# Kernel tuning notes

Hardware: AMD Instinct MI355X
Metric: run time of the kernel (lower is better)

Reference implementation:

```python
import jax, jax.numpy as jnp
import numpy as np

BIG = 1e30  # stands in for sys.maxsize in fp32-safe form


def _find_neg_anchors(e_actv, host):
    # Full pairwise Euclidean distance matrix (equivalent to the
    # pdist -> triangular reconstruction in the torch code).
    sq = jnp.sum(e_actv * e_actv, axis=1)                       # [n]
    d2 = sq[:, None] + sq[None, :] - 2.0 * (e_actv @ e_actv.T)  # [n, n]
    dist = jnp.sqrt(jnp.maximum(d2, 0.0))
    n = e_actv.shape[0]
    # mask: self (diagonal) and same-discriminator pairs -> huge distance
    same_discr = host[:, None] == host[None, :]
    eye = jnp.eye(n, dtype=bool)
    dist = jnp.where(same_discr | eye, BIG, dist)
    idxs = jnp.argmin(dist, axis=1)                             # [n]
    return e_actv[idxs]                                         # gather


def setup_inputs() -> dict:
    key = jax.random.key(0)
    k1, k2, k3 = jax.random.split(key, 3)
    n, d = 8192, 256
    e_actv = jax.random.normal(k1, (n, d), dtype=jnp.float32)
    e_ap = jax.random.normal(k2, (n, d), dtype=jnp.float32)
    host = jax.random.randint(k3, (n,), 0, 64, dtype=jnp.int64 if jax.config.read('jax_enable_x64') else jnp.int32)
    return {"e_actv": e_actv, "e_ap": e_ap, "host": host}


def reference(e_actv, e_ap, host):
    # forward returns (e_actv, e_ap, e_an); e_an computed under no_grad
    e_an = jax.lax.stop_gradient(_find_neg_anchors(e_actv, host))
    return (e_actv, e_ap, e_an)
```

## Files before the change

kernel.cpp:

```cpp
#include <hip/hip_runtime.h>
#include <hip/hip_bf16.h>
#include <cmath>
#include <cstddef>

#define N 8192
#define D 256
#define BI 128
#define NT (N / BI)
#define NTRI (NT * (NT + 1) / 2)

typedef __attribute__((ext_vector_type(8))) short short8;
typedef __attribute__((ext_vector_type(4))) float float4v;

__device__ inline ushort f2bf(float x) {
    __hip_bfloat16 h = __float2bfloat16(x);
    return __builtin_bit_cast(ushort, h);
}
__device__ inline float bf2f(ushort u) {
    __hip_bfloat16 h = __builtin_bit_cast(__hip_bfloat16, u);
    return __bfloat162float(h);
}

__device__ inline unsigned long long packKI(float k, int idx) {
    unsigned u = __float_as_uint(k);
    u = (u & 0x80000000u) ? ~u : (u | 0x80000000u);
    return ((unsigned long long)u << 32) | (unsigned)idx;
}

__device__ inline int triT(int t) { return t * (129 - t) / 2; }


__global__ void prep_kernel(const float4* __restrict__ a, const float4* __restrict__ p,
                            float4* __restrict__ out, float* __restrict__ sq,
                            ushort* __restrict__ Ehi, ushort* __restrict__ Elo,
                            unsigned long long* __restrict__ M) {
    const int gsz = gridDim.x * blockDim.x;
    const int g0 = blockIdx.x * blockDim.x + threadIdx.x;
    const int total = N * D / 4;

    for (int idx = g0; idx < total; idx += gsz) {
        float4 v = a[idx];
        out[idx] = v;
        float s = v.x * v.x + v.y * v.y + v.z * v.z + v.w * v.w;
        #pragma unroll
        for (int off = 32; off; off >>= 1) s += __shfl_down(s, off);
        if ((threadIdx.x & 63) == 0) sq[idx >> 6] = s;
    }
    for (int idx = g0; idx < total; idx += gsz) out[total + idx] = p[idx];

    {
        const int w = g0 >> 6;
        if (w < 4096) {
            const int lane = threadIdx.x & 63;
            const int tx = lane & 15;
            const int q  = lane >> 4;
            const int r16 = w >> 3;
            const int ktc = w & 7;
            const int row = r16 * 16 + tx;
            const float4 v0 = a[row * 64 + ktc * 8 + q * 2];
            const float4 v1 = a[row * 64 + ktc * 8 + q * 2 + 1];
            float e[8] = {v0.x, v0.y, v0.z, v0.w, v1.x, v1.y, v1.z, v1.w};
            short8 hs, ls;
            #pragma unroll
            for (int j = 0; j < 8; j++) {
                ushort h = f2bf(e[j]);
                ushort l = f2bf(e[j] - bf2f(h));
                hs[j] = (short)h;
                ls[j] = (short)l;
            }
            const size_t off = (size_t)(r16 * 8 + ktc) * 512 + lane * 8;
            *(short8*)&Ehi[off] = hs;
            *(short8*)&Elo[off] = ls;
        }
    }
    for (int i = g0; i < N; i += gsz) M[i] = 0xFFFFFFFFFFFFFFFFull;
}

__launch_bounds__(256, 2)
__global__ void argmin_sym(const ushort* __restrict__ Ehi, const ushort* __restrict__ Elo,
                           const int* __restrict__ host, const float* __restrict__ sq,
                           unsigned long long* __restrict__ M) {
    const int b0 = blockIdx.x;
    const int b = (b0 & 7) * (NTRI / 8) + (b0 >> 3);
    int ti = (int)floor(64.5 - sqrt(64.5 * 64.5 - 2.0 * (double)b));
    while (triT(ti + 1) <= b) ti++;
    while (triT(ti) > b) ti--;
    const int tj = ti + (b - triT(ti));

    __shared__ float sqA_s[BI], sqB_s[BI];
    __shared__ int   hostB_s[BI];
    __shared__ float rowV[2 * BI]; __shared__ int rowI[2 * BI];
    __shared__ float colV[2 * BI]; __shared__ int colI[2 * BI];

    const int ib0 = ti * BI;
    const int jb0 = tj * BI;
    const int tid = threadIdx.x;
    const int lane = tid & 63;
    const int wave = tid >> 6;
    const int wrow = wave >> 1;
    const int wcol = wave & 1;
    const int tx = lane & 15;
    const int q  = lane >> 4;

    if (tid < BI) {
        sqA_s[tid] = sq[ib0 + tid];
        sqB_s[tid] = sq[jb0 + tid];
        hostB_s[tid] = host[jb0 + tid];
    }

    unsigned hostAp[4];
    #pragma unroll
    for (int rt = 0; rt < 4; rt++) {
        unsigned p = 0;
        #pragma unroll
        for (int reg = 0; reg < 4; reg++) {
            int hv = host[ib0 + wrow * 64 + rt * 16 + q * 4 + reg];
            p |= ((unsigned)hv & 0xFFu) << (8 * reg);
        }
        hostAp[rt] = p;
    }

    float4v acc[4][4];
    #pragma unroll
    for (int rt = 0; rt < 4; rt++)
        #pragma unroll
        for (int ct = 0; ct < 4; ct++) acc[rt][ct] = (float4v)(0.0f);

    const int pA = (ib0 >> 4) + wrow * 4;
    const int pB = (jb0 >> 4) + wcol * 4;
    const int lo8 = lane * 8;

    #pragma unroll
    for (int ktc = 0; ktc < 8; ktc++) {
        short8 ah[4], al[4], bh[4], bl[4];
        #pragma unroll
        for (int rt = 0; rt < 4; rt++) {
            const int o = ((pA + rt) * 8 + ktc) * 512 + lo8;
            ah[rt] = *(const short8*)&Ehi[o];
            al[rt] = *(const short8*)&Elo[o];
        }
        #pragma unroll
        for (int ct = 0; ct < 4; ct++) {
            const int o = ((pB + ct) * 8 + ktc) * 512 + lo8;
            bh[ct] = *(const short8*)&Ehi[o];
            bl[ct] = *(const short8*)&Elo[o];
        }
        #pragma unroll
        for (int rt = 0; rt < 4; rt++)
            #pragma unroll
            for (int ct = 0; ct < 4; ct++)
                acc[rt][ct] = __builtin_amdgcn_mfma_f32_16x16x32_bf16(ah[rt], bh[ct], acc[rt][ct], 0, 0, 0);
        #pragma unroll
        for (int rt = 0; rt < 4; rt++)
            #pragma unroll
            for (int ct = 0; ct < 4; ct++)
                acc[rt][ct] = __builtin_amdgcn_mfma_f32_16x16x32_bf16(ah[rt], bl[ct], acc[rt][ct], 0, 0, 0);
        #pragma unroll
        for (int rt = 0; rt < 4; rt++)
            #pragma unroll
            for (int ct = 0; ct < 4; ct++)
                acc[rt][ct] = __builtin_amdgcn_mfma_f32_16x16x32_bf16(al[rt], bh[ct], acc[rt][ct], 0, 0, 0);
    }

    __syncthreads();

    #pragma unroll
    for (int rt = 0; rt < 4; rt++) {
        unsigned hp = hostAp[rt];
        #pragma unroll
        for (int reg = 0; reg < 4; reg++) {
            int il = wrow * 64 + rt * 16 + q * 4 + reg;
            int ig = ib0 + il;
            int ha = (int)((hp >> (8 * reg)) & 0xFFu);
            float v = 3.0e38f; int ix = 0x7fffffff;
            #pragma unroll
            for (int ct = 0; ct < 4; ct++) {
                int jl = wcol * 64 + ct * 16 + tx;
                int jg = jb0 + jl;
                float key = sqB_s[jl] - 2.0f * acc[rt][ct][reg];
                bool masked = (hostB_s[jl] == ha) || (jg == ig);
                if (!masked && (key < v || (key == v && jg < ix))) { v = key; ix = jg; }
            }
            #pragma unroll
            for (int d = 1; d < 16; d <<= 1) {
                float ov = __shfl_xor(v, d);
                int   oi = __shfl_xor(ix, d);
                if (ov < v || (ov == v && oi < ix)) { v = ov; ix = oi; }
            }
            if (tx == 0) { rowV[il * 2 + wcol] = v; rowI[il * 2 + wcol] = ix; }
        }
    }

    if (ti != tj) {
        #pragma unroll
        for (int ct = 0; ct < 4; ct++) {
            int jl = wcol * 64 + ct * 16 + tx;
            int hb = hostB_s[jl];
            float v = 3.0e38f; int ix = 0x7fffffff;
            #pragma unroll
            for (int rt = 0; rt < 4; rt++) {
                unsigned hp = hostAp[rt];
                #pragma unroll
                for (int reg = 0; reg < 4; reg++) {
                    int il = wrow * 64 + rt * 16 + q * 4 + reg;
                    int ig = ib0 + il;
                    bool masked = ((int)((hp >> (8 * reg)) & 0xFFu) == hb);
                    float key = sqA_s[il] - 2.0f * acc[rt][ct][reg];
                    if (!masked && (key < v || (key == v && ig < ix))) { v = key; ix = ig; }
                }
            }
            #pragma unroll
            for (int d = 16; d < 64; d <<= 1) {
                float ov = __shfl_xor(v, d);
                int   oi = __shfl_xor(ix, d);
                if (ov < v || (ov == v && oi < ix)) { v = ov; ix = oi; }
            }
            if (q == 0) { colV[jl * 2 + wrow] = v; colI[jl * 2 + wrow] = ix; }
        }
    }

    __syncthreads();
    if (tid < BI) {
        float v0 = rowV[tid * 2];     int x0 = rowI[tid * 2];
        float v1 = rowV[tid * 2 + 1]; int x1 = rowI[tid * 2 + 1];
        if (v1 < v0 || (v1 == v0 && x1 < x0)) { v0 = v1; x0 = x1; }
        atomicMin(&M[ib0 + tid], packKI(v0, x0));
        if (ti != tj) {
            float w0 = colV[tid * 2];     int y0 = colI[tid * 2];
            float w1 = colV[tid * 2 + 1]; int y1 = colI[tid * 2 + 1];
            if (w1 < w0 || (w1 == w0 && y1 < y0)) { w0 = w1; y0 = y1; }
            atomicMin(&M[jb0 + tid], packKI(w0, y0));
        }
    }
}

__global__ void finalize_kernel(const unsigned long long* __restrict__ M,
                                const float* __restrict__ E, float* __restrict__ out_an) {
    int row = blockIdx.x;
    int t = threadIdx.x;
    int idx = (int)(unsigned)(M[row] & 0xFFFFFFFFull);
    float4 v = *(const float4*)&E[(size_t)idx * D + t * 4];
    *(float4*)&out_an[(size_t)row * D + t * 4] = v;
}

extern "C" void kernel_launch(void* const* d_in, const int* in_sizes, int n_in,
                              void* d_out, int out_size, void* d_ws, size_t ws_size,
                              hipStream_t stream) {
    const float* e_actv = (const float*)d_in[0];
    const float* e_ap   = (const float*)d_in[1];
    const int*   host   = (const int*)d_in[2];
    float* out = (float*)d_out;

    unsigned long long* M = (unsigned long long*)d_ws;
    float*  sq  = (float*)(M + N);
    ushort* Ehi = (ushort*)(sq + N);
    ushort* Elo = Ehi + (size_t)N * D;

    prep_kernel<<<1024, 256, 0, stream>>>(
        (const float4*)e_actv, (const float4*)e_ap, (float4*)out,
        sq, Ehi, Elo, M);
    argmin_sym<<<NTRI, 256, 0, stream>>>(Ehi, Elo, host, sq, M);
    finalize_kernel<<<N, 64, 0, stream>>>(M, e_actv, out + 2 * (size_t)N * D);
}
```

Before: 185.3 us.

## Software-pipeline global fragment loads ahead of MFMA issue in Gram loop

```diff
diff --git a/kernel.cpp b/kernel.cpp
--- a/kernel.cpp
+++ b/kernel.cpp
@@ -130,36 +130,47 @@
     const int pB = (jb0 >> 4) + wcol * 4;
     const int lo8 = lane * 8;
 
-    #pragma unroll
-    for (int ktc = 0; ktc < 8; ktc++) {
-        short8 ah[4], al[4], bh[4], bl[4];
-        #pragma unroll
-        for (int rt = 0; rt < 4; rt++) {
-            const int o = ((pA + rt) * 8 + ktc) * 512 + lo8;
-            ah[rt] = *(const short8*)&Ehi[o];
-            al[rt] = *(const short8*)&Elo[o];
-        }
+    short8 aH[3], aL[3];
+    short8 bhv[2][4], blv[2][4];
+
+    auto loadA = [&](int s) {
+        const int k = s >> 2, rt = s & 3, sl = s % 3;
+        const int o = ((pA + rt) * 8 + k) * 512 + lo8;
+        aH[sl] = *(const short8*)&Ehi[o];
+        aL[sl] = *(const short8*)&Elo[o];
+    };
+    auto loadB = [&](int k) {
+        const int p = k & 1;
         #pragma unroll
         for (int ct = 0; ct < 4; ct++) {
-            const int o = ((pB + ct) * 8 + ktc) * 512 + lo8;
-            bh[ct] = *(const short8*)&Ehi[o];
-            bl[ct] = *(const short8*)&Elo[o];
-        }
-        #pragma unroll
-        for (int rt = 0; rt < 4; rt++)
-            #pragma unroll
-            for (int ct = 0; ct < 4; ct++)
-                acc[rt][ct] = __builtin_amdgcn_mfma_f32_16x16x32_bf16(ah[rt], bh[ct], acc[rt][ct], 0, 0, 0);
-        #pragma unroll
-        for (int rt = 0; rt < 4; rt++)
-            #pragma unroll
-            for (int ct = 0; ct < 4; ct++)
-                acc[rt][ct] = __builtin_amdgcn_mfma_f32_16x16x32_bf16(ah[rt], bl[ct], acc[rt][ct], 0, 0, 0);
-        #pragma unroll
-        for (int rt = 0; rt < 4; rt++)
-            #pragma unroll
-            for (int ct = 0; ct < 4; ct++)
-                acc[rt][ct] = __builtin_amdgcn_mfma_f32_16x16x32_bf16(al[rt], bh[ct], acc[rt][ct], 0, 0, 0);
+            const int o = ((pB + ct) * 8 + k) * 512 + lo8;
+            bhv[p][ct] = *(const short8*)&Ehi[o];
+            blv[p][ct] = *(const short8*)&Elo[o];
+        }
+    };
+
+    loadB(0);
+    loadA(0);
+    loadA(1);
+
+    #pragma unroll
+    for (int s = 0; s < 32; s++) {
+        const int k = s >> 2;
+        const int rt = s & 3;
+        const int sl = s % 3;
+        const int p = k & 1;
+        if (rt == 0 && k < 7) loadB(k + 1);
+        if (s + 2 < 32) loadA(s + 2);
+        __builtin_amdgcn_sched_barrier(0);
+        #pragma unroll
+        for (int ct = 0; ct < 4; ct++)
+            acc[rt][ct] = __builtin_amdgcn_mfma_f32_16x16x32_bf16(aH[sl], bhv[p][ct], acc[rt][ct], 0, 0, 0);
+        #pragma unroll
+        for (int ct = 0; ct < 4; ct++)
+            acc[rt][ct] = __builtin_amdgcn_mfma_f32_16x16x32_bf16(aH[sl], blv[p][ct], acc[rt][ct], 0, 0, 0);
+        #pragma unroll
+        for (int ct = 0; ct < 4; ct++)
+            acc[rt][ct] = __builtin_amdgcn_mfma_f32_16x16x32_bf16(aL[sl], bhv[p][ct], acc[rt][ct], 0, 0, 0);
     }
 
     __syncthreads();
```

Result: no change. 188.0 us (+1.5%).

## Use 128x64 upper-triangular tiles with double-buffered operand loads

Applied to the files above, without the earlier changes.

```diff
diff --git a/kernel.cpp b/kernel.cpp
--- a/kernel.cpp
+++ b/kernel.cpp
@@ -5,9 +5,10 @@
 
 #define N 8192
 #define D 256
-#define BI 128
-#define NT (N / BI)
-#define NTRI (NT * (NT + 1) / 2)
+#define BIR 128
+#define BJC 64
+#define NBI (N / BIR)
+#define NBLK 4160
 
 typedef __attribute__((ext_vector_type(8))) short short8;
 typedef __attribute__((ext_vector_type(4))) float float4v;
@@ -27,7 +28,7 @@
     return ((unsigned long long)u << 32) | (unsigned)idx;
 }
 
-__device__ inline int triT(int t) { return t * (129 - t) / 2; }
+__device__ inline int bandS(int t) { return t * (129 - t); }
 
 
 __global__ void prep_kernel(const float4* __restrict__ a, const float4* __restrict__ p,
@@ -76,24 +77,25 @@
     for (int i = g0; i < N; i += gsz) M[i] = 0xFFFFFFFFFFFFFFFFull;
 }
 
-__launch_bounds__(256, 2)
+__launch_bounds__(256, 3)
 __global__ void argmin_sym(const ushort* __restrict__ Ehi, const ushort* __restrict__ Elo,
                            const int* __restrict__ host, const float* __restrict__ sq,
                            unsigned long long* __restrict__ M) {
     const int b0 = blockIdx.x;
-    const int b = (b0 & 7) * (NTRI / 8) + (b0 >> 3);
-    int ti = (int)floor(64.5 - sqrt(64.5 * 64.5 - 2.0 * (double)b));
-    while (triT(ti + 1) <= b) ti++;
-    while (triT(ti) > b) ti--;
-    const int tj = ti + (b - triT(ti));
-
-    __shared__ float sqA_s[BI], sqB_s[BI];
-    __shared__ int   hostB_s[BI];
-    __shared__ float rowV[2 * BI]; __shared__ int rowI[2 * BI];
-    __shared__ float colV[2 * BI]; __shared__ int colI[2 * BI];
-
-    const int ib0 = ti * BI;
-    const int jb0 = tj * BI;
+    const int b = (b0 & 7) * (NBLK / 8) + (b0 >> 3);
+    int ti = (int)floor((129.0 - sqrt(129.0 * 129.0 - 4.0 * (double)b)) * 0.5);
+    while (bandS(ti + 1) <= b) ti++;
+    while (bandS(ti) > b) ti--;
+    const int tj = 2 * ti + (b - bandS(ti));
+
+    __shared__ float sqA_s[BIR];
+    __shared__ float sqB_s[BJC];
+    __shared__ int   hostB_s[BJC];
+    __shared__ float rowV[2 * BIR]; __shared__ int rowI[2 * BIR];
+    __shared__ float colV[2 * BJC]; __shared__ int colI[2 * BJC];
+
+    const int ib0 = ti * BIR;
+    const int jb0 = tj * BJC;
     const int tid = threadIdx.x;
     const int lane = tid & 63;
     const int wave = tid >> 6;
@@ -102,8 +104,8 @@
     const int tx = lane & 15;
     const int q  = lane >> 4;
 
-    if (tid < BI) {
-        sqA_s[tid] = sq[ib0 + tid];
+    if (tid < BIR) sqA_s[tid] = sq[ib0 + tid];
+    if (tid < BJC) {
         sqB_s[tid] = sq[jb0 + tid];
         hostB_s[tid] = host[jb0 + tid];
     }
@@ -120,46 +122,58 @@
         hostAp[rt] = p;
     }
 
-    float4v acc[4][4];
+    float4v acc[4][2];
     #pragma unroll
     for (int rt = 0; rt < 4; rt++)
         #pragma unroll
-        for (int ct = 0; ct < 4; ct++) acc[rt][ct] = (float4v)(0.0f);
+        for (int ct = 0; ct < 2; ct++) acc[rt][ct] = (float4v)(0.0f);
 
     const int pA = (ib0 >> 4) + wrow * 4;
-    const int pB = (jb0 >> 4) + wcol * 4;
+    const int pB = (jb0 >> 4) + wcol * 2;
     const int lo8 = lane * 8;
 
-    #pragma unroll
-    for (int ktc = 0; ktc < 8; ktc++) {
-        short8 ah[4], al[4], bh[4], bl[4];
+    short8 aH[2][4], aL[2][4], bH[2][2], bL[2][2];
+
+    auto loadChunk = [&](int k) {
+        const int s = k & 1;
         #pragma unroll
         for (int rt = 0; rt < 4; rt++) {
-            const int o = ((pA + rt) * 8 + ktc) * 512 + lo8;
-            ah[rt] = *(const short8*)&Ehi[o];
-            al[rt] = *(const short8*)&Elo[o];
-        }
-        #pragma unroll
-        for (int ct = 0; ct < 4; ct++) {
-            const int o = ((pB + ct) * 8 + ktc) * 512 + lo8;
-            bh[ct] = *(const short8*)&Ehi[o];
-            bl[ct] = *(const short8*)&Elo[o];
-        }
+            const int o = ((pA + rt) * 8 + k) * 512 + lo8;
+            aH[s][rt] = *(const short8*)&Ehi[o];
+            aL[s][rt] = *(const short8*)&Elo[o];
+        }
+        #pragma unroll
+        for (int ct = 0; ct < 2; ct++) {
+            const int o = ((pB + ct) * 8 + k) * 512 + lo8;
+            bH[s][ct] = *(const short8*)&Ehi[o];
+            bL[s][ct] = *(const short8*)&Elo[o];
+        }
+    };
+
+    loadChunk(0);
+    loadChunk(1);
+
+    #pragma unroll
+    for (int k = 0; k < 8; k++) {
+        const int s = k & 1;
+        __builtin_amdgcn_sched_barrier(0);
         #pragma unroll
         for (int rt = 0; rt < 4; rt++)
             #pragma unroll
-            for (int ct = 0; ct < 4; ct++)
-                acc[rt][ct] = __builtin_amdgcn_mfma_f32_16x16x32_bf16(ah[rt], bh[ct], acc[rt][ct], 0, 0, 0);
+            for (int ct = 0; ct < 2; ct++)
+                acc[rt][ct] = __builtin_amdgcn_mfma_f32_16x16x32_bf16(aH[s][rt], bH[s][ct], acc[rt][ct], 0, 0, 0);
         #pragma unroll
         for (int rt = 0; rt < 4; rt++)
             #pragma unroll
-            for (int ct = 0; ct < 4; ct++)
-                acc[rt][ct] = __builtin_amdgcn_mfma_f32_16x16x32_bf16(ah[rt], bl[ct], acc[rt][ct], 0, 0, 0);
+            for (int ct = 0; ct < 2; ct++)
+                acc[rt][ct] = __builtin_amdgcn_mfma_f32_16x16x32_bf16(aH[s][rt], bL[s][ct], acc[rt][ct], 0, 0, 0);
         #pragma unroll
         for (int rt = 0; rt < 4; rt++)
             #pragma unroll
-            for (int ct = 0; ct < 4; ct++)
-                acc[rt][ct] = __builtin_amdgcn_mfma_f32_16x16x32_bf16(al[rt], bh[ct], acc[rt][ct], 0, 0, 0);
+            for (int ct = 0; ct < 2; ct++)
+                acc[rt][ct] = __builtin_amdgcn_mfma_f32_16x16x32_bf16(aL[s][rt], bH[s][ct], acc[rt][ct], 0, 0, 0);
+        __builtin_amdgcn_sched_barrier(0);
+        if (k + 2 < 8) loadChunk(k + 2);
     }
 
     __syncthreads();
@@ -174,11 +188,11 @@
             int ha = (int)((hp >> (8 * reg)) & 0xFFu);
             float v = 3.0e38f; int ix = 0x7fffffff;
             #pragma unroll
-            for (int ct = 0; ct < 4; ct++) {
-                int jl = wcol * 64 + ct * 16 + tx;
+            for (int ct = 0; ct < 2; ct++) {
+                int jl = wcol * 32 + ct * 16 + tx;
                 int jg = jb0 + jl;
                 float key = sqB_s[jl] - 2.0f * acc[rt][ct][reg];
-                bool masked = (hostB_s[jl] == ha) || (jg == ig);
+                bool masked = (hostB_s[jl] == ha) || (jg <= ig);
                 if (!masked && (key < v || (key == v && jg < ix))) { v = key; ix = jg; }
             }
             #pragma unroll
@@ -191,46 +205,45 @@
         }
     }
 
-    if (ti != tj) {
-        #pragma unroll
-        for (int ct = 0; ct < 4; ct++) {
-            int jl = wcol * 64 + ct * 16 + tx;
-            int hb = hostB_s[jl];
-            float v = 3.0e38f; int ix = 0x7fffffff;
-            #pragma unroll
-            for (int rt = 0; rt < 4; rt++) {
-                unsigned hp = hostAp[rt];
-                #pragma unroll
-                for (int reg = 0; reg < 4; reg++) {
-                    int il = wrow * 64 + rt * 16 + q * 4 + reg;
-                    int ig = ib0 + il;
-                    bool masked = ((int)((hp >> (8 * reg)) & 0xFFu) == hb);
-                    float key = sqA_s[il] - 2.0f * acc[rt][ct][reg];
-                    if (!masked && (key < v || (key == v && ig < ix))) { v = key; ix = ig; }
-                }
-            }
-            #pragma unroll
-            for (int d = 16; d < 64; d <<= 1) {
-                float ov = __shfl_xor(v, d);
-                int   oi = __shfl_xor(ix, d);
-                if (ov < v || (ov == v && oi < ix)) { v = ov; ix = oi; }
-            }
-            if (q == 0) { colV[jl * 2 + wrow] = v; colI[jl * 2 + wrow] = ix; }
-        }
+    #pragma unroll
+    for (int ct = 0; ct < 2; ct++) {
+        int jl = wcol * 32 + ct * 16 + tx;
+        int jg = jb0 + jl;
+        int hb = hostB_s[jl];
+        float v = 3.0e38f; int ix = 0x7fffffff;
+        #pragma unroll
+        for (int rt = 0; rt < 4; rt++) {
+            unsigned hp = hostAp[rt];
+            #pragma unroll
+            for (int reg = 0; reg < 4; reg++) {
+                int il = wrow * 64 + rt * 16 + q * 4 + reg;
+                int ig = ib0 + il;
+                bool masked = ((int)((hp >> (8 * reg)) & 0xFFu) == hb) || (ig >= jg);
+                float key = sqA_s[il] - 2.0f * acc[rt][ct][reg];
+                if (!masked && (key < v || (key == v && ig < ix))) { v = key; ix = ig; }
+            }
+        }
+        #pragma unroll
+        for (int d = 16; d < 64; d <<= 1) {
+            float ov = __shfl_xor(v, d);
+            int   oi = __shfl_xor(ix, d);
+            if (ov < v || (ov == v && oi < ix)) { v = ov; ix = oi; }
+        }
+        if (q == 0) { colV[jl * 2 + wrow] = v; colI[jl * 2 + wrow] = ix; }
     }
 
     __syncthreads();
-    if (tid < BI) {
+    if (tid < BIR) {
         float v0 = rowV[tid * 2];     int x0 = rowI[tid * 2];
         float v1 = rowV[tid * 2 + 1]; int x1 = rowI[tid * 2 + 1];
         if (v1 < v0 || (v1 == v0 && x1 < x0)) { v0 = v1; x0 = x1; }
         atomicMin(&M[ib0 + tid], packKI(v0, x0));
-        if (ti != tj) {
-            float w0 = colV[tid * 2];     int y0 = colI[tid * 2];
-            float w1 = colV[tid * 2 + 1]; int y1 = colI[tid * 2 + 1];
-            if (w1 < w0 || (w1 == w0 && y1 < y0)) { w0 = w1; y0 = y1; }
-            atomicMin(&M[jb0 + tid], packKI(w0, y0));
-        }
+    }
+    if (tid < BJC) {
+        float w0 = colV[tid * 2];     int y0 = colI[tid * 2];
+        float w1 = colV[tid * 2 + 1]; int y1 = colI[tid * 2 + 1];
+        if (w1 < w0 || (w1 == w0 && y1 < y0)) { w0 = w1; y0 = y1; }
+        atomicMin(&M[jb0 + tid], packKI(w0, y0));
     }
 }
 
@@ -259,6 +272,6 @@
     prep_kernel<<<1024, 256, 0, stream>>>(
         (const float4*)e_actv, (const float4*)e_ap, (float4*)out,
         sq, Ehi, Elo, M);
-    argmin_sym<<<NTRI, 256, 0, stream>>>(Ehi, Elo, host, sq, M);
+    argmin_sym<<<NBLK, 256, 0, stream>>>(Ehi, Elo, host, sq, M);
     finalize_kernel<<<N, 64, 0, stream>>>(M, e_actv, out + 2 * (size_t)N * D);
 }
```

After: 182.1 us. Within noise of the previous version (-1.7%).

## Restructure symmetric argmin into 64-row strips over four column tiles with register-resident A

Applied to the files above, without the earlier changes.

```diff
diff --git a/kernel.cpp b/kernel.cpp
--- a/kernel.cpp
+++ b/kernel.cpp
@@ -5,12 +5,14 @@
 
 #define N 8192
 #define D 256
-#define BI 128
-#define NT (N / BI)
-#define NTRI (NT * (NT + 1) / 2)
+#define NBB 128
+#define JT 4
+#define NBLK2 2112
 
 typedef __attribute__((ext_vector_type(8))) short short8;
 typedef __attribute__((ext_vector_type(4))) float float4v;
+
+#define U64MAX 0xFFFFFFFFFFFFFFFFull
 
 __device__ inline ushort f2bf(float x) {
     __hip_bfloat16 h = __float2bfloat16(x);
@@ -26,8 +28,11 @@
     u = (u & 0x80000000u) ? ~u : (u | 0x80000000u);
     return ((unsigned long long)u << 32) | (unsigned)idx;
 }
-
-__device__ inline int triT(int t) { return t * (129 - t) / 2; }
+__device__ inline unsigned long long min64(unsigned long long a, unsigned long long b) {
+    return a < b ? a : b;
+}
+
+__device__ inline int segG(int n) { int a = n >> 2, r = n & 3; return 2 * a * (a + 1) + r * (a + 1); }
 
 
 __global__ void prep_kernel(const float4* __restrict__ a, const float4* __restrict__ p,
@@ -76,161 +81,144 @@
     for (int i = g0; i < N; i += gsz) M[i] = 0xFFFFFFFFFFFFFFFFull;
 }
 
-__launch_bounds__(256, 2)
+__launch_bounds__(256, 3)
 __global__ void argmin_sym(const ushort* __restrict__ Ehi, const ushort* __restrict__ Elo,
                            const int* __restrict__ host, const float* __restrict__ sq,
                            unsigned long long* __restrict__ M) {
     const int b0 = blockIdx.x;
-    const int b = (b0 & 7) * (NTRI / 8) + (b0 >> 3);
-    int ti = (int)floor(64.5 - sqrt(64.5 * 64.5 - 2.0 * (double)b));
-    while (triT(ti + 1) <= b) ti++;
-    while (triT(ti) > b) ti--;
-    const int tj = ti + (b - triT(ti));
-
-    __shared__ float sqA_s[BI], sqB_s[BI];
-    __shared__ int   hostB_s[BI];
-    __shared__ float rowV[2 * BI]; __shared__ int rowI[2 * BI];
-    __shared__ float colV[2 * BI]; __shared__ int colI[2 * BI];
-
-    const int ib0 = ti * BI;
-    const int jb0 = tj * BI;
+    const int b = (b0 & 7) * (NBLK2 / 8) + (b0 >> 3);
+    int bb = 0;
+    while (bb < 127 && (NBLK2 - segG(NBB - (bb + 1))) <= b) bb++;
+    const int seg = b - (NBLK2 - segG(NBB - bb));
+    const int tj0 = bb + 4 * seg;
+    const int ntiles = min(JT, NBB - tj0);
+    const int jr0 = tj0 * 64;
+
+    __shared__ float sqB_s[256];
+    __shared__ int   hostB_s[256];
+    __shared__ unsigned long long colV[4][256];
+
     const int tid = threadIdx.x;
     const int lane = tid & 63;
-    const int wave = tid >> 6;
-    const int wrow = wave >> 1;
-    const int wcol = wave & 1;
+    const int w = tid >> 6;
     const int tx = lane & 15;
     const int q  = lane >> 4;
 
-    if (tid < BI) {
-        sqA_s[tid] = sq[ib0 + tid];
-        sqB_s[tid] = sq[jb0 + tid];
-        hostB_s[tid] = host[jb0 + tid];
-    }
-
-    unsigned hostAp[4];
-    #pragma unroll
-    for (int rt = 0; rt < 4; rt++) {
-        unsigned p = 0;
-        #pragma unroll
-        for (int reg = 0; reg < 4; reg++) {
-            int hv = host[ib0 + wrow * 64 + rt * 16 + q * 4 + reg];
-            p |= ((unsigned)hv & 0xFFu) << (8 * reg);
-        }
-        hostAp[rt] = p;
-    }
-
-    float4v acc[4][4];
-    #pragma unroll
-    for (int rt = 0; rt < 4; rt++)
-        #pragma unroll
-        for (int ct = 0; ct < 4; ct++) acc[rt][ct] = (float4v)(0.0f);
-
-    const int pA = (ib0 >> 4) + wrow * 4;
-    const int pB = (jb0 >> 4) + wcol * 4;
+    const int ig0 = bb * 64 + w * 16;
+    const int rg  = bb * 4 + w;
     const int lo8 = lane * 8;
 
-    #pragma unroll
-    for (int ktc = 0; ktc < 8; ktc++) {
-        short8 ah[4], al[4], bh[4], bl[4];
-        #pragma unroll
-        for (int rt = 0; rt < 4; rt++) {
-            const int o = ((pA + rt) * 8 + ktc) * 512 + lo8;
-            ah[rt] = *(const short8*)&Ehi[o];
-            al[rt] = *(const short8*)&Elo[o];
-        }
+    short8 bH[2][4], bL[2][4];
+    auto loadB = [&](int slot, int tj, int k) {
         #pragma unroll
         for (int ct = 0; ct < 4; ct++) {
-            const int o = ((pB + ct) * 8 + ktc) * 512 + lo8;
-            bh[ct] = *(const short8*)&Ehi[o];
-            bl[ct] = *(const short8*)&Elo[o];
-        }
-        #pragma unroll
-        for (int rt = 0; rt < 4; rt++)
+            const int o = ((tj * 4 + ct) * 8 + k) * 512 + lo8;
+            bH[slot][ct] = *(const short8*)&Ehi[o];
+            bL[slot][ct] = *(const short8*)&Elo[o];
+        }
+    };
+    loadB(0, tj0, 0);
+
+    short8 aH[8], aL[8];
+    #pragma unroll
+    for (int k = 0; k < 8; k++) {
+        const int o = (rg * 8 + k) * 512 + lo8;
+        aH[k] = *(const short8*)&Ehi[o];
+        aL[k] = *(const short8*)&Elo[o];
+    }
+
+    float sqA[4];
+    unsigned hostAp = 0;
+    #pragma unroll
+    for (int reg = 0; reg < 4; reg++) {
+        const int ig = ig0 + q * 4 + reg;
+        sqA[reg] = sq[ig];
+        hostAp |= ((unsigned)host[ig] & 0xFFu) << (8 * reg);
+    }
+
+    {
+        const int jcl = min(jr0 + tid, N - 1);
+        if (tid < 256) {
+            sqB_s[tid] = sq[jcl];
+            hostB_s[tid] = host[jcl];
+            #pragma unroll
+            for (int i = 0; i < 4; i++) colV[i][tid] = U64MAX;
+        }
+    }
+    __syncthreads();
+
+    unsigned long long rmin[4] = {U64MAX, U64MAX, U64MAX, U64MAX};
+
+    float4v acc[4];
+    #pragma unroll
+    for (int ct = 0; ct < 4; ct++) acc[ct] = (float4v)(0.0f);
+
+    for (int it = 0; it < ntiles; ++it) {
+        const int tj = tj0 + it;
+        const bool diag = (it == 0) && (seg == 0);
+
+        #pragma unroll
+        for (int k = 0; k < 8; k++) {
+            const int slot = k & 1;
+            if (k < 7) loadB(slot ^ 1, tj, k + 1);
+            else if (it + 1 < ntiles) loadB(slot ^ 1, tj + 1, 0);
+            __builtin_amdgcn_sched_barrier(0);
             #pragma unroll
             for (int ct = 0; ct < 4; ct++)
-                acc[rt][ct] = __builtin_amdgcn_mfma_f32_16x16x32_bf16(ah[rt], bh[ct], acc[rt][ct], 0, 0, 0);
-        #pragma unroll
-        for (int rt = 0; rt < 4; rt++)
+                acc[ct] = __builtin_amdgcn_mfma_f32_16x16x32_bf16(aH[k], bH[slot][ct], acc[ct], 0, 0, 0);
             #pragma unroll
             for (int ct = 0; ct < 4; ct++)
-                acc[rt][ct] = __builtin_amdgcn_mfma_f32_16x16x32_bf16(ah[rt], bl[ct], acc[rt][ct], 0, 0, 0);
-        #pragma unroll
-        for (int rt = 0; rt < 4; rt++)
+                acc[ct] = __builtin_amdgcn_mfma_f32_16x16x32_bf16(aH[k], bL[slot][ct], acc[ct], 0, 0, 0);
             #pragma unroll
             for (int ct = 0; ct < 4; ct++)
-                acc[rt][ct] = __builtin_amdgcn_mfma_f32_16x16x32_bf16(al[rt], bh[ct], acc[rt][ct], 0, 0, 0);
+                acc[ct] = __builtin_amdgcn_mfma_f32_16x16x32_bf16(aL[k], bH[slot][ct], acc[ct], 0, 0, 0);
+        }
+
+        #pragma unroll
+        for (int ct = 0; ct < 4; ct++) {
+            const int jl = it * 64 + ct * 16 + tx;
+            const int jg = jr0 + jl;
+            const float sb = sqB_s[jl];
+            const int   hb = hostB_s[jl];
+            unsigned long long cm = U64MAX;
+            #pragma unroll
+            for (int reg = 0; reg < 4; reg++) {
+                const int ig = ig0 + q * 4 + reg;
+                const int ha = (int)((hostAp >> (8 * reg)) & 0xFFu);
+                const float d = acc[ct][reg];
+                const bool masked = (hb == ha) || (diag && (jg <= ig));
+                const float rkey = fmaf(-2.0f, d, sb);
+                const float ckey = fmaf(-2.0f, d, sqA[reg]);
+                const unsigned long long rp = masked ? U64MAX : packKI(rkey, jg);
+                const unsigned long long cp = masked ? U64MAX : packKI(ckey, ig);
+                rmin[reg] = min64(rmin[reg], rp);
+                cm = min64(cm, cp);
+            }
+            cm = min64(cm, (unsigned long long)__shfl_xor((unsigned long long)cm, 16));
+            cm = min64(cm, (unsigned long long)__shfl_xor((unsigned long long)cm, 32));
+            if (q == 0) colV[w][jl] = cm;
+        }
+        #pragma unroll
+        for (int ct = 0; ct < 4; ct++) acc[ct] = (float4v)(0.0f);
+    }
+
+    #pragma unroll
+    for (int reg = 0; reg < 4; reg++) {
+        #pragma unroll
+        for (int d = 1; d < 16; d <<= 1)
+            rmin[reg] = min64(rmin[reg], (unsigned long long)__shfl_xor((unsigned long long)rmin[reg], d));
+    }
+    if (tx == 0) {
+        #pragma unroll
+        for (int reg = 0; reg < 4; reg++)
+            atomicMin(&M[ig0 + q * 4 + reg], rmin[reg]);
     }
 
     __syncthreads();
-
-    #pragma unroll
-    for (int rt = 0; rt < 4; rt++) {
-        unsigned hp = hostAp[rt];
-        #pragma unroll
-        for (int reg = 0; reg < 4; reg++) {
-            int il = wrow * 64 + rt * 16 + q * 4 + reg;
-            int ig = ib0 + il;
-            int ha = (int)((hp >> (8 * reg)) & 0xFFu);
-            float v = 3.0e38f; int ix = 0x7fffffff;
-            #pragma unroll
-            for (int ct = 0; ct < 4; ct++) {
-                int jl = wcol * 64 + ct * 16 + tx;
-                int jg = jb0 + jl;
-                float key = sqB_s[jl] - 2.0f * acc[rt][ct][reg];
-                bool masked = (hostB_s[jl] == ha) || (jg == ig);
-                if (!masked && (key < v || (key == v && jg < ix))) { v = key; ix = jg; }
-            }
-            #pragma unroll
-            for (int d = 1; d < 16; d <<= 1) {
-                float ov = __shfl_xor(v, d);
-                int   oi = __shfl_xor(ix, d);
-                if (ov < v || (ov == v && oi < ix)) { v = ov; ix = oi; }
-            }
-            if (tx == 0) { rowV[il * 2 + wcol] = v; rowI[il * 2 + wcol] = ix; }
-        }
-    }
-
-    if (ti != tj) {
-        #pragma unroll
-        for (int ct = 0; ct < 4; ct++) {
-            int jl = wcol * 64 + ct * 16 + tx;
-            int hb = hostB_s[jl];
-            float v = 3.0e38f; int ix = 0x7fffffff;
-            #pragma unroll
-            for (int rt = 0; rt < 4; rt++) {
-                unsigned hp = hostAp[rt];
-                #pragma unroll
-                for (int reg = 0; reg < 4; reg++) {
-                    int il = wrow * 64 + rt * 16 + q * 4 + reg;
-                    int ig = ib0 + il;
-                    bool masked = ((int)((hp >> (8 * reg)) & 0xFFu) == hb);
-                    float key = sqA_s[il] - 2.0f * acc[rt][ct][reg];
-                    if (!masked && (key < v || (key == v && ig < ix))) { v = key; ix = ig; }
-                }
-            }
-            #pragma unroll
-            for (int d = 16; d < 64; d <<= 1) {
-                float ov = __shfl_xor(v, d);
-                int   oi = __shfl_xor(ix, d);
-                if (ov < v || (ov == v && oi < ix)) { v = ov; ix = oi; }
-            }
-            if (q == 0) { colV[jl * 2 + wrow] = v; colI[jl * 2 + wrow] = ix; }
-        }
-    }
-
-    __syncthreads();
-    if (tid < BI) {
-        float v0 = rowV[tid * 2];     int x0 = rowI[tid * 2];
-        float v1 = rowV[tid * 2 + 1]; int x1 = rowI[tid * 2 + 1];
-        if (v1 < v0 || (v1 == v0 && x1 < x0)) { v0 = v1; x0 = x1; }
-        atomicMin(&M[ib0 + tid], packKI(v0, x0));
-        if (ti != tj) {
-            float w0 = colV[tid * 2];     int y0 = colI[tid * 2];
-            float w1 = colV[tid * 2 + 1]; int y1 = colI[tid * 2 + 1];
-            if (w1 < w0 || (w1 == w0 && y1 < y0)) { w0 = w1; y0 = y1; }
-            atomicMin(&M[jb0 + tid], packKI(w0, y0));
-        }
+    if (tid < ntiles * 64) {
+        unsigned long long m = min64(min64(colV[0][tid], colV[1][tid]),
+                                     min64(colV[2][tid], colV[3][tid]));
+        atomicMin(&M[jr0 + tid], m);
     }
 }
 
@@ -259,6 +247,6 @@
     prep_kernel<<<1024, 256, 0, stream>>>(
         (const float4*)e_actv, (const float4*)e_ap, (float4*)out,
         sq, Ehi, Elo, M);
-    argmin_sym<<<NTRI, 256, 0, stream>>>(Ehi, Elo, host, sq, M);
+    argmin_sym<<<NBLK2, 256, 0, stream>>>(Ehi, Elo, host, sq, M);
     finalize_kernel<<<N, 64, 0, stream>>>(M, e_actv, out + 2 * (size_t)N * D);
 }
```

After: 225.8 us. 21.8% more time.
